# Kernel tuning notes

Measured on AMD Instinct MI355X. Metric: run time of the kernel, lower is better.

## Reference

```python
import jax, jax.numpy as jnp
import numpy as np

HIDDEN = 2048
N_HEADS = 32
N_KV = 4
HEAD_DIM = 128
EPS = 1e-6
THETA = 1e6
B, S = 2, 2048


def setup_inputs() -> dict:
    key = jax.random.key(0)
    k1, k2, k3 = jax.random.split(key, 3)
    hidden_states = jax.random.normal(k1, (B, S, HIDDEN), dtype=jnp.float32)
    positions = jnp.broadcast_to(jnp.arange(S, dtype=jnp.int32), (B, S))
    w_qkv = jax.random.normal(k2, ((N_HEADS + 2 * N_KV) * HEAD_DIM, HIDDEN), dtype=jnp.float32) * 0.02
    w_o = jax.random.normal(k3, (HIDDEN, N_HEADS * HEAD_DIM), dtype=jnp.float32) * 0.02
    q_norm_w = jnp.ones((HEAD_DIM,), dtype=jnp.float32)
    k_norm_w = jnp.ones((HEAD_DIM,), dtype=jnp.float32)
    return {"hidden_states": hidden_states, "positions": positions,
            "w_qkv": w_qkv, "w_o": w_o, "q_norm_w": q_norm_w, "k_norm_w": k_norm_w}


def _rms_norm(x, w):
    # x: [..., HEAD_DIM]
    var = jnp.mean(x * x, axis=-1, keepdims=True)
    return x * jax.lax.rsqrt(var + EPS) * w


def _rope(x, positions):
    # NEOX-style rotary. x: [B,S,H,D], positions: [B,S]
    half = HEAD_DIM // 2
    inv_freq = 1.0 / (THETA ** (jnp.arange(0, half, dtype=jnp.float32) / half))
    ang = positions.astype(jnp.float32)[..., None] * inv_freq  # [B,S,half]
    cos = jnp.cos(ang)[:, :, None, :]
    sin = jnp.sin(ang)[:, :, None, :]
    x1, x2 = x[..., :half], x[..., half:]
    return jnp.concatenate([x1 * cos - x2 * sin, x2 * cos + x1 * sin], axis=-1)


def reference(hidden_states, positions, w_qkv, w_o, q_norm_w, k_norm_w):
    q_size = N_HEADS * HEAD_DIM
    kv_size = N_KV * HEAD_DIM
    qkv = jnp.einsum('bsh,oh->bso', hidden_states, w_qkv)
    q = qkv[..., :q_size].reshape(B, S, N_HEADS, HEAD_DIM)
    k = qkv[..., q_size:q_size + kv_size].reshape(B, S, N_KV, HEAD_DIM)
    v = qkv[..., q_size + kv_size:].reshape(B, S, N_KV, HEAD_DIM)
    # per-head RMSNorm then RoPE
    q = _rope(_rms_norm(q, q_norm_w), positions)
    k = _rope(_rms_norm(k, k_norm_w), positions)
    rep = N_HEADS // N_KV
    k = jnp.repeat(k, rep, axis=2)
    v = jnp.repeat(v, rep, axis=2)
    scale = HEAD_DIM ** -0.5
    scores = jnp.einsum('bqhd,bkhd->bhqk', q, k) * scale
    causal = jnp.tril(jnp.ones((S, S), dtype=bool))
    scores = jnp.where(causal, scores, jnp.finfo(scores.dtype).min)
    probs = jax.nn.softmax(scores, axis=-1)
    attn = jnp.einsum('bhqk,bkhd->bqhd', probs, v).reshape(B, S, N_HEADS * HEAD_DIM)
    return jnp.einsum('bsa,ha->bsh', attn, w_o)
```

## Files before the change

### kernel.cpp

```cpp
#include <hip/hip_runtime.h>
#include <cstdint>

#define SEQ 2048
#define BATCH 2
#define NTOK 4096
#define HID 2048
#define NH 32
#define NKV 4
#define HD 128
#define QKV_O 5120

typedef __attribute__((ext_vector_type(8))) short short8;
typedef __attribute__((ext_vector_type(8))) unsigned short u16x8;
typedef __attribute__((ext_vector_type(4))) unsigned short u16x4;
typedef __attribute__((ext_vector_type(4))) float f32x4;

__device__ __forceinline__ float bf2f(unsigned short u) {
  union { unsigned int i; float f; } v; v.i = ((unsigned int)u) << 16; return v.f;
}
__device__ __forceinline__ unsigned short f2bf(float f) {
  union { float f; unsigned int i; } v; v.f = f;
  unsigned int r = v.i + 0x7FFFu + ((v.i >> 16) & 1u);
  return (unsigned short)(r >> 16);
}

__device__ __forceinline__ void load_lds16(const void* g, void* l) {
  __builtin_amdgcn_global_load_lds((const __attribute__((address_space(1))) unsigned int*)g,
                                   (__attribute__((address_space(3))) unsigned int*)l, 16, 0, 0);
}

__global__ __launch_bounds__(256) void convert_to_bf16(const float* __restrict__ src,
                                                       unsigned short* __restrict__ dst,
                                                       int n4) {
  int i = blockIdx.x * blockDim.x + threadIdx.x;
  int stride = gridDim.x * blockDim.x;
  for (; i < n4; i += stride) {
    f32x4 v = *(const f32x4*)(src + 4 * (size_t)i);
    u16x4 o;
    o.x = f2bf(v.x); o.y = f2bf(v.y); o.z = f2bf(v.z); o.w = f2bf(v.w);
    *(u16x4*)(dst + 4 * (size_t)i) = o;
  }
}

template <bool OUT_F32>
__global__ __launch_bounds__(256) void gemm_bt_bf16(
    const unsigned short* __restrict__ A, const unsigned short* __restrict__ B,
    void* __restrict__ Cv, int lda, int ldb, int ldc, int K) {
  __shared__ alignas(16) unsigned short As[128 * 32];
  __shared__ alignas(16) unsigned short Bs[128 * 32];

  const int t    = threadIdx.x;
  const int lane = t & 63;
  const int w    = t >> 6;
  const int wm   = (w >> 1) * 64;
  const int wn   = (w & 1) * 64;
  const size_t m0 = (size_t)blockIdx.y * 128;
  const size_t n0 = (size_t)blockIdx.x * 128;

  f32x4 acc[4][4] = {};

  const int srow = w * 32 + (lane >> 2);
  const int scol = (lane & 3) * 8;
  const unsigned short* gA0 = &A[(m0 + srow) * (size_t)lda + scol];
  const unsigned short* gA1 = gA0 + 16 * (size_t)lda;
  const unsigned short* gB0 = &B[(n0 + srow) * (size_t)ldb + scol];
  const unsigned short* gB1 = gB0 + 16 * (size_t)ldb;
  unsigned short* lA0 = &As[(w * 32) * 32];
  unsigned short* lA1 = &As[(w * 32 + 16) * 32];
  unsigned short* lB0 = &Bs[(w * 32) * 32];
  unsigned short* lB1 = &Bs[(w * 32 + 16) * 32];

  const int fr = lane & 15;
  const int kb = (lane >> 4) * 8;

  for (int k0 = 0; k0 < K; k0 += 32) {
    load_lds16(gA0 + k0, lA0);
    load_lds16(gA1 + k0, lA1);
    load_lds16(gB0 + k0, lB0);
    load_lds16(gB1 + k0, lB1);
    __syncthreads();
    short8 af[4], bf[4];
#pragma unroll
    for (int mt = 0; mt < 4; mt++) af[mt] = *(const short8*)&As[(wm + mt * 16 + fr) * 32 + kb];
#pragma unroll
    for (int nt = 0; nt < 4; nt++) bf[nt] = *(const short8*)&Bs[(wn + nt * 16 + fr) * 32 + kb];
#pragma unroll
    for (int mt = 0; mt < 4; mt++)
#pragma unroll
      for (int nt = 0; nt < 4; nt++)
        acc[mt][nt] = __builtin_amdgcn_mfma_f32_16x16x32_bf16(af[mt], bf[nt], acc[mt][nt], 0, 0, 0);
    __syncthreads();
  }

  const int r4 = (lane >> 4) * 4;
  const int cc = lane & 15;
#pragma unroll
  for (int mt = 0; mt < 4; mt++)
#pragma unroll
    for (int nt = 0; nt < 4; nt++) {
      size_t row = m0 + wm + mt * 16 + r4;
      size_t col = n0 + wn + nt * 16 + cc;
#pragma unroll
      for (int r = 0; r < 4; r++) {
        if (OUT_F32) ((float*)Cv)[(row + r) * ldc + col] = acc[mt][nt][r];
        else ((unsigned short*)Cv)[(row + r) * ldc + col] = f2bf(acc[mt][nt][r]);
      }
    }
}

__global__ __launch_bounds__(64) void normrope(
    unsigned short* __restrict__ qkv, const int* __restrict__ pos,
    const unsigned short* __restrict__ qw, const unsigned short* __restrict__ kw) {
  const int h    = blockIdx.x;
  const int tok  = blockIdx.z * SEQ + blockIdx.y;
  const int lane = threadIdx.x;

  const unsigned short* w = (h < NH) ? qw : kw;
  const size_t src = (size_t)tok * QKV_O + (size_t)h * HD;

  float x1 = bf2f(qkv[src + lane]);
  float x2 = bf2f(qkv[src + lane + 64]);
  float ss = x1 * x1 + x2 * x2;
#pragma unroll
  for (int off = 32; off; off >>= 1) ss += __shfl_xor(ss, off);
  float r = rsqrtf(ss * (1.0f / 128.0f) + 1e-6f);
  float n1 = x1 * r * bf2f(w[lane]);
  float n2 = x2 * r * bf2f(w[lane + 64]);

  float p = (float)pos[tok];
  float inv_freq = expf((float)lane * (-13.815510557964274f / 64.0f));
  float ang = p * inv_freq;
  float c = cosf(ang), s = sinf(ang);
  qkv[src + lane]      = f2bf(n1 * c - n2 * s);
  qkv[src + lane + 64] = f2bf(n2 * c + n1 * s);
}

__global__ __launch_bounds__(256) void transpose_v(const unsigned short* __restrict__ qkv,
                                                   unsigned short* __restrict__ vt) {
  __shared__ alignas(16) unsigned short Vs[64][136];
  const int k0 = blockIdx.x * 64, kvh = blockIdx.y, b = blockIdx.z;
  const int t = threadIdx.x;
  const int voff = (NH + NKV) * HD + kvh * HD;
  {
    const int row = t >> 2, cb = (t & 3) * 8;
    const size_t gb = (size_t)(b * SEQ + k0 + row) * QKV_O + voff;
#pragma unroll
    for (int r = 0; r < 4; r++)
      *(uint4*)&Vs[row][cb + 32 * r] = *(const uint4*)&qkv[gb + cb + 32 * r];
  }
  __syncthreads();
  const int d = t >> 1, half = t & 1;
  const size_t ob = ((size_t)((b * NKV + kvh) * HD + d)) * SEQ + k0 + half * 32;
#pragma unroll
  for (int i = 0; i < 4; i++) {
    u16x8 vv;
#pragma unroll
    for (int j = 0; j < 8; j++) vv[j] = Vs[half * 32 + i * 8 + j][d];
    *(u16x8*)&vt[ob + i * 8] = vv;
  }
}

__global__ __launch_bounds__(512, 4) void flash_mfma(unsigned short* __restrict__ qkv,
                                                     const unsigned short* __restrict__ vt) {
  __shared__ alignas(16) unsigned short Kbuf[2][64 * 128];
  __shared__ alignas(16) unsigned short Vbuf[2][128 * 64];
  __shared__ alignas(16) unsigned short Ps[8][16 * 64];

  const int p = (int)blockIdx.x;
  const int h = blockIdx.y, b = blockIdx.z;
  const int t = threadIdx.x;
  const int lane = t & 63, w = t >> 6;
  const int c = lane & 15, g = lane >> 4;
  const int kvh = h >> 3;
  const int koff = NH * HD + kvh * HD;
  const float scale = 0.08838834764831845f;
  const int swz = c & 7;
  const int nqt = SEQ / 128;

  const int rK0 = t >> 4,         jK0 = (t & 15) ^ (rK0 & 7);
  const int rK1 = (t + 512) >> 4, jK1 = ((t + 512) & 15) ^ (rK1 & 7);
  const int dV0 = t >> 3,         jV0 = (t & 7) ^ (dV0 & 7);
  const int dV1 = (t + 512) >> 3, jV1 = ((t + 512) & 7) ^ (dV1 & 7);
  const unsigned short* gK0 = qkv + (size_t)(b * SEQ + rK0) * QKV_O + koff + jK0 * 8;
  const unsigned short* gK1 = qkv + (size_t)(b * SEQ + rK1) * QKV_O + koff + jK1 * 8;
  const unsigned short* gV0 = vt + ((size_t)(b * NKV + kvh) * HD + dV0) * SEQ + jV0 * 8;
  const unsigned short* gV1 = vt + ((size_t)(b * NKV + kvh) * HD + dV1) * SEQ + jV1 * 8;

  auto stage = [&](int k0s, int bi) {
    load_lds16(gK0 + (size_t)k0s * QKV_O, &Kbuf[bi][(w * 64) * 8]);
    load_lds16(gK1 + (size_t)k0s * QKV_O, &Kbuf[bi][(w * 64 + 512) * 8]);
    load_lds16(gV0 + k0s, &Vbuf[bi][(w * 64) * 8]);
    load_lds16(gV1 + k0s, &Vbuf[bi][(w * 64 + 512) * 8]);
  };

  for (int job = 0; job < 2; job++) {
    const int qt = job == 0 ? (nqt - 1 - p) : p;
    const int q0 = qt * 128;
    const int nkt = 2 * qt + 2;

    stage(0, 0);

    short8 qf[4];
    {
      const size_t qrow = (size_t)(b * SEQ + q0 + w * 16 + c) * QKV_O + (size_t)h * HD;
#pragma unroll
      for (int ks = 0; ks < 4; ks++)
        qf[ks] = *(const short8*)&qkv[qrow + ks * 32 + g * 8];
    }

    f32x4 O[8] = {};
    float m_i = -1e30f, l_i = 0.0f;

    for (int kt = 0; kt < nkt; kt++) {
      const int cur = kt & 1;
      asm volatile("s_waitcnt vmcnt(0)" ::: "memory");
      __builtin_amdgcn_s_barrier();
      __builtin_amdgcn_sched_barrier(0);
      if (kt + 1 < nkt) stage((kt + 1) * 64, cur ^ 1);

      const unsigned short* Kc = Kbuf[cur];
      const unsigned short* Vc = Vbuf[cur];

      f32x4 sc[4];
#pragma unroll
      for (int mt = 0; mt < 4; mt++) sc[mt] = (f32x4){0.f, 0.f, 0.f, 0.f};
      __builtin_amdgcn_s_setprio(1);
#pragma unroll
      for (int ks = 0; ks < 4; ks++) {
#pragma unroll
        for (int mt = 0; mt < 4; mt++) {
          short8 kf = *(const short8*)&Kc[(mt * 16 + c) * 128 + (((ks * 4 + g) ^ swz) * 8)];
          sc[mt] = __builtin_amdgcn_mfma_f32_16x16x32_bf16(kf, qf[ks], sc[mt], 0, 0, 0);
        }
      }
      __builtin_amdgcn_s_setprio(0);

      const int k0 = kt * 64;
      const int qrow = q0 + w * 16 + c;
      const bool need_mask = (k0 + 63 > q0 + w * 16);
      float mx = -1e30f;
#pragma unroll
      for (int mt = 0; mt < 4; mt++)
#pragma unroll
        for (int r = 0; r < 4; r++) {
          float s = sc[mt][r] * scale;
          if (need_mask && (k0 + mt * 16 + g * 4 + r > qrow)) s = -1e30f;
          sc[mt][r] = s;
          mx = fmaxf(mx, s);
        }
      mx = fmaxf(mx, __shfl_xor(mx, 16));
      mx = fmaxf(mx, __shfl_xor(mx, 32));
      float m_new = fmaxf(m_i, mx);
      float alpha = __expf(m_i - m_new);
      float psum = 0.0f;
#pragma unroll
      for (int mt = 0; mt < 4; mt++) {
        u16x4 p4;
#pragma unroll
        for (int r = 0; r < 4; r++) {
          float pv = __expf(sc[mt][r] - m_new);
          psum += pv;
          p4[r] = f2bf(pv);
        }
        *(u16x4*)&Ps[w][c * 64 + (((mt * 2 + (g >> 1)) ^ swz) * 8) + (g & 1) * 4] = p4;
      }
      psum += __shfl_xor(psum, 16);
      psum += __shfl_xor(psum, 32);
      l_i = l_i * alpha + psum;
      m_i = m_new;

      f32x4 a4;
#pragma unroll
      for (int r = 0; r < 4; r++) a4[r] = __shfl(alpha, g * 4 + r);
#pragma unroll
      for (int nt = 0; nt < 8; nt++)
#pragma unroll
        for (int r = 0; r < 4; r++) O[nt][r] *= a4[r];

      __builtin_amdgcn_s_setprio(1);
#pragma unroll
      for (int ks = 0; ks < 2; ks++) {
        short8 pf = *(const short8*)&Ps[w][c * 64 + (((ks * 4 + g) ^ swz) * 8)];
#pragma unroll
        for (int nt = 0; nt < 8; nt++) {
          short8 vf = *(const short8*)&Vc[(nt * 16 + c) * 64 + (((ks * 4 + g) ^ swz) * 8)];
          O[nt] = __builtin_amdgcn_mfma_f32_16x16x32_bf16(pf, vf, O[nt], 0, 0, 0);
        }
      }
      __builtin_amdgcn_s_setprio(0);
    }

    f32x4 l4;
#pragma unroll
    for (int r = 0; r < 4; r++) l4[r] = __shfl(l_i, g * 4 + r);
    f32x4 li;
#pragma unroll
    for (int r = 0; r < 4; r++) li[r] = 1.0f / l4[r];
#pragma unroll
    for (int nt = 0; nt < 8; nt++)
#pragma unroll
      for (int r = 0; r < 4; r++) {
        size_t addr = (size_t)(b * SEQ + q0 + w * 16 + g * 4 + r) * QKV_O + h * HD + nt * 16 + c;
        qkv[addr] = f2bf(O[nt][r] * li[r]);
      }
  }
}

extern "C" void kernel_launch(void* const* d_in, const int* in_sizes, int n_in,
                              void* d_out, int out_size, void* d_ws, size_t ws_size,
                              hipStream_t stream) {
  const float* hidden_f = (const float*)d_in[0];
  const int* positions  = (const int*)d_in[1];
  const float* wqkv_f   = (const float*)d_in[2];
  const float* wo_f     = (const float*)d_in[3];
  const float* qn_f     = (const float*)d_in[4];
  const float* kn_f     = (const float*)d_in[5];
  float* out            = (float*)d_out;

  char* ws = (char*)d_ws;
  unsigned short* hidden_c = (unsigned short*)ws;
  unsigned short* wqkv_c   = (unsigned short*)(ws + 16777216);
  unsigned short* wo_c     = (unsigned short*)(ws + 37748736);
  unsigned short* qn_c     = (unsigned short*)(ws + 54525952);
  unsigned short* kn_c     = (unsigned short*)(ws + 54526208);
  unsigned short* qkv      = (unsigned short*)(ws + 54526464);
  unsigned short* vt_g     = (unsigned short*)(ws + 96469504);

  convert_to_bf16<<<1024, 256, 0, stream>>>(hidden_f, hidden_c, NTOK * HID / 4);
  convert_to_bf16<<<1024, 256, 0, stream>>>(wqkv_f, wqkv_c, QKV_O * HID / 4);
  convert_to_bf16<<<1024, 256, 0, stream>>>(wo_f, wo_c, HID * NH * HD / 4);
  convert_to_bf16<<<1, 32, 0, stream>>>(qn_f, qn_c, HD / 4);
  convert_to_bf16<<<1, 32, 0, stream>>>(kn_f, kn_c, HD / 4);

  gemm_bt_bf16<false><<<dim3(QKV_O / 128, NTOK / 128), 256, 0, stream>>>(
      hidden_c, wqkv_c, qkv, HID, HID, QKV_O, HID);
  normrope<<<dim3(NH + NKV, SEQ, BATCH), 64, 0, stream>>>(qkv, positions, qn_c, kn_c);
  transpose_v<<<dim3(SEQ / 64, NKV, BATCH), 256, 0, stream>>>(qkv, vt_g);
  flash_mfma<<<dim3(SEQ / 256, NH, BATCH), 512, 0, stream>>>(qkv, vt_g);
  gemm_bt_bf16<true><<<dim3(HID / 128, NTOK / 128), 256, 0, stream>>>(
      qkv, wo_c, out, QKV_O, NH * HD, HID, NH * HD);
}
```

Before: 541.5 us.

## Precompute RoPE table, widen normrope blocks, lazy softmax rescale, full K swizzle

```diff
diff --git a/kernel.cpp b/kernel.cpp
--- a/kernel.cpp
+++ b/kernel.cpp
@@ -108,12 +108,24 @@
     }
 }
 
-__global__ __launch_bounds__(64) void normrope(
-    unsigned short* __restrict__ qkv, const int* __restrict__ pos,
+__global__ __launch_bounds__(64) void rope_tab(const int* __restrict__ pos,
+                                               float2* __restrict__ tab) {
+  const int tok = blockIdx.x;
+  const int j = threadIdx.x;
+  float p = (float)pos[tok];
+  float inv_freq = expf((float)j * (-13.815510557964274f / 64.0f));
+  float ang = p * inv_freq;
+  float2 cs; cs.x = cosf(ang); cs.y = sinf(ang);
+  tab[tok * 64 + j] = cs;
+}
+
+__global__ __launch_bounds__(256) void normrope(
+    unsigned short* __restrict__ qkv, const float2* __restrict__ tab,
     const unsigned short* __restrict__ qw, const unsigned short* __restrict__ kw) {
-  const int h    = blockIdx.x;
+  const int wv   = threadIdx.x >> 6;
+  const int lane = threadIdx.x & 63;
+  const int h    = blockIdx.x * 4 + wv;
   const int tok  = blockIdx.z * SEQ + blockIdx.y;
-  const int lane = threadIdx.x;
 
   const unsigned short* w = (h < NH) ? qw : kw;
   const size_t src = (size_t)tok * QKV_O + (size_t)h * HD;
@@ -127,12 +139,9 @@
   float n1 = x1 * r * bf2f(w[lane]);
   float n2 = x2 * r * bf2f(w[lane + 64]);
 
-  float p = (float)pos[tok];
-  float inv_freq = expf((float)lane * (-13.815510557964274f / 64.0f));
-  float ang = p * inv_freq;
-  float c = cosf(ang), s = sinf(ang);
-  qkv[src + lane]      = f2bf(n1 * c - n2 * s);
-  qkv[src + lane + 64] = f2bf(n2 * c + n1 * s);
+  float2 cs = tab[tok * 64 + lane];
+  qkv[src + lane]      = f2bf(n1 * cs.x - n2 * cs.y);
+  qkv[src + lane + 64] = f2bf(n2 * cs.x + n1 * cs.y);
 }
 
 __global__ __launch_bounds__(256) void transpose_v(const unsigned short* __restrict__ qkv,
@@ -177,8 +186,8 @@
   const int swz = c & 7;
   const int nqt = SEQ / 128;
 
-  const int rK0 = t >> 4,         jK0 = (t & 15) ^ (rK0 & 7);
-  const int rK1 = (t + 512) >> 4, jK1 = ((t + 512) & 15) ^ (rK1 & 7);
+  const int rK0 = t >> 4,         jK0 = (t & 15) ^ (rK0 & 15);
+  const int rK1 = (t + 512) >> 4, jK1 = ((t + 512) & 15) ^ (rK1 & 15);
   const int dV0 = t >> 3,         jV0 = (t & 7) ^ (dV0 & 7);
   const int dV1 = (t + 512) >> 3, jV1 = ((t + 512) & 7) ^ (dV1 & 7);
   const unsigned short* gK0 = qkv + (size_t)(b * SEQ + rK0) * QKV_O + koff + jK0 * 8;
@@ -202,10 +211,10 @@
 
     short8 qf[4];
     {
-      const size_t qrow = (size_t)(b * SEQ + q0 + w * 16 + c) * QKV_O + (size_t)h * HD;
+      const size_t qr = (size_t)(b * SEQ + q0 + w * 16 + c) * QKV_O + (size_t)h * HD;
 #pragma unroll
       for (int ks = 0; ks < 4; ks++)
-        qf[ks] = *(const short8*)&qkv[qrow + ks * 32 + g * 8];
+        qf[ks] = *(const short8*)&qkv[qr + ks * 32 + g * 8];
     }
 
     f32x4 O[8] = {};
@@ -229,7 +238,7 @@
       for (int ks = 0; ks < 4; ks++) {
 #pragma unroll
         for (int mt = 0; mt < 4; mt++) {
-          short8 kf = *(const short8*)&Kc[(mt * 16 + c) * 128 + (((ks * 4 + g) ^ swz) * 8)];
+          short8 kf = *(const short8*)&Kc[(mt * 16 + c) * 128 + (((ks * 4 + g) ^ c) * 8)];
           sc[mt] = __builtin_amdgcn_mfma_f32_16x16x32_bf16(kf, qf[ks], sc[mt], 0, 0, 0);
         }
       }
@@ -238,27 +247,41 @@
       const int k0 = kt * 64;
       const int qrow = q0 + w * 16 + c;
       const bool need_mask = (k0 + 63 > q0 + w * 16);
-      float mx = -1e30f;
+      float mx = -3.0e38f;
 #pragma unroll
       for (int mt = 0; mt < 4; mt++)
 #pragma unroll
         for (int r = 0; r < 4; r++) {
-          float s = sc[mt][r] * scale;
-          if (need_mask && (k0 + mt * 16 + g * 4 + r > qrow)) s = -1e30f;
+          float s = sc[mt][r];
+          if (need_mask && (k0 + mt * 16 + g * 4 + r > qrow)) s = -3.0e38f;
           sc[mt][r] = s;
           mx = fmaxf(mx, s);
         }
       mx = fmaxf(mx, __shfl_xor(mx, 16));
       mx = fmaxf(mx, __shfl_xor(mx, 32));
-      float m_new = fmaxf(m_i, mx);
-      float alpha = __expf(m_i - m_new);
+      float mxs = mx * scale;
+
+      if (!__all(mxs - m_i <= 8.0f)) {
+        float m_new = fmaxf(m_i, mxs);
+        float alpha = __expf(m_i - m_new);
+        f32x4 a4;
+#pragma unroll
+        for (int r = 0; r < 4; r++) a4[r] = __shfl(alpha, g * 4 + r);
+#pragma unroll
+        for (int nt = 0; nt < 8; nt++)
+#pragma unroll
+          for (int r = 0; r < 4; r++) O[nt][r] *= a4[r];
+        l_i *= alpha;
+        m_i = m_new;
+      }
+
       float psum = 0.0f;
 #pragma unroll
       for (int mt = 0; mt < 4; mt++) {
         u16x4 p4;
 #pragma unroll
         for (int r = 0; r < 4; r++) {
-          float pv = __expf(sc[mt][r] - m_new);
+          float pv = __expf(__builtin_fmaf(sc[mt][r], scale, -m_i));
           psum += pv;
           p4[r] = f2bf(pv);
         }
@@ -266,16 +289,7 @@
       }
       psum += __shfl_xor(psum, 16);
       psum += __shfl_xor(psum, 32);
-      l_i = l_i * alpha + psum;
-      m_i = m_new;
-
-      f32x4 a4;
-#pragma unroll
-      for (int r = 0; r < 4; r++) a4[r] = __shfl(alpha, g * 4 + r);
-#pragma unroll
-      for (int nt = 0; nt < 8; nt++)
-#pragma unroll
-        for (int r = 0; r < 4; r++) O[nt][r] *= a4[r];
+      l_i += psum;
 
       __builtin_amdgcn_s_setprio(1);
 #pragma unroll
@@ -325,6 +339,7 @@
   unsigned short* kn_c     = (unsigned short*)(ws + 54526208);
   unsigned short* qkv      = (unsigned short*)(ws + 54526464);
   unsigned short* vt_g     = (unsigned short*)(ws + 96469504);
+  float2* rtab             = (float2*)ws;
 
   convert_to_bf16<<<1024, 256, 0, stream>>>(hidden_f, hidden_c, NTOK * HID / 4);
   convert_to_bf16<<<1024, 256, 0, stream>>>(wqkv_f, wqkv_c, QKV_O * HID / 4);
@@ -334,7 +349,8 @@
 
   gemm_bt_bf16<false><<<dim3(QKV_O / 128, NTOK / 128), 256, 0, stream>>>(
       hidden_c, wqkv_c, qkv, HID, HID, QKV_O, HID);
-  normrope<<<dim3(NH + NKV, SEQ, BATCH), 64, 0, stream>>>(qkv, positions, qn_c, kn_c);
+  rope_tab<<<NTOK, 64, 0, stream>>>(positions, rtab);
+  normrope<<<dim3((NH + NKV) / 4, SEQ, BATCH), 256, 0, stream>>>(qkv, rtab, qn_c, kn_c);
   transpose_v<<<dim3(SEQ / 64, NKV, BATCH), 256, 0, stream>>>(qkv, vt_g);
   flash_mfma<<<dim3(SEQ / 256, NH, BATCH), 512, 0, stream>>>(qkv, vt_g);
   gemm_bt_bf16<true><<<dim3(HID / 128, NTOK / 128), 256, 0, stream>>>(
```

Measured after the change: 505.0 us. -6.7%, faster.
